# Kernel tuning notes

Measured on AMD Instinct MI355X. Metric: run time of the kernel, lower is better.

## Reference

```python
import jax, jax.numpy as jnp
import numpy as np

N = 50000      # nodes
E = 600000     # message-passing edges (avg degree 12)
P = 500000     # candidate pairs
DH = 128       # d_h
NRBF = 16      # n_rbf
NL = 3         # n_layers
RBF_MAX = 1.5  # coords in [0,1]^2 -> max dist sqrt(2) ~ 1.414


def _mlp2(x, W1, b1, W2, b2):
    # mlp([a, b, c]) = Linear(a,b) -> ReLU -> Linear(b,c); dropout=0.0 is a no-op
    return jnp.dot(jax.nn.relu(jnp.dot(x, W1) + b1), W2) + b2


def _rbf(r):
    # Gaussian radial basis expansion of edge distances, NRBF centers on [0, RBF_MAX]
    centers = jnp.linspace(0.0, RBF_MAX, NRBF, dtype=r.dtype)
    width = centers[1] - centers[0]
    return jnp.exp(-jnp.square((r[:, None] - centers) / width))


def setup_inputs() -> dict:
    key = jax.random.key(0)
    ks = jax.random.split(key, 24)

    def lin(k, fan_in, fan_out):
        return jax.random.normal(k, (fan_in, fan_out), dtype=jnp.float32) / np.sqrt(fan_in)

    def lin_stack(k, n, fan_in, fan_out):
        return jax.random.normal(k, (n, fan_in, fan_out), dtype=jnp.float32) / np.sqrt(fan_in)

    inp = {}
    inp["coords01"] = jax.random.uniform(ks[0], (N, 2), dtype=jnp.float32)
    inp["msg_edge_index"] = jax.random.randint(ks[1], (2, E), 0, N)
    inp["cand_pairs_uv"] = jax.random.randint(ks[2], (P, 2), 0, N)
    # node_in: mlp([2, DH, DH])
    inp["node_W1"] = lin(ks[3], 2, DH)
    inp["node_b1"] = jnp.zeros((DH,), jnp.float32)
    inp["node_W2"] = lin(ks[4], DH, DH)
    inp["node_b2"] = jnp.zeros((DH,), jnp.float32)
    # per-layer InvariantMPNN params, stacked over NL layers
    # message MLP: [2*DH + NRBF, DH, DH]
    inp["msg_W1"] = lin_stack(ks[5], NL, 2 * DH + NRBF, DH)
    inp["msg_b1"] = jnp.zeros((NL, DH), jnp.float32)
    inp["msg_W2"] = lin_stack(ks[6], NL, DH, DH)
    inp["msg_b2"] = jnp.zeros((NL, DH), jnp.float32)
    # update MLP: [2*DH, DH, DH]
    inp["upd_W1"] = lin_stack(ks[7], NL, 2 * DH, DH)
    inp["upd_b1"] = jnp.zeros((NL, DH), jnp.float32)
    inp["upd_W2"] = lin_stack(ks[8], NL, DH, DH)
    inp["upd_b2"] = jnp.zeros((NL, DH), jnp.float32)
    # edge head: mlp([2*DH + 1, DH, 1])
    inp["head_W1"] = lin(ks[9], 2 * DH + 1, DH)
    inp["head_b1"] = jnp.zeros((DH,), jnp.float32)
    inp["head_W2"] = lin(ks[10], DH, 1)
    inp["head_b2"] = jnp.zeros((1,), jnp.float32)
    return inp


def reference(coords01, node_W1, node_b1, node_W2, node_b2,
              msg_W1, msg_b1, msg_W2, msg_b2,
              upd_W1, upd_b1, upd_W2, upd_b2,
              head_W1, head_b1, head_W2, head_b2,
              msg_edge_index, cand_pairs_uv):
    # node embedding from 2D coordinates
    h = _mlp2(coords01, node_W1, node_b1, node_W2, node_b2)  # [N, DH]

    src = msg_edge_index[0]
    dst = msg_edge_index[1]
    dx = coords01[src] - coords01[dst]                       # [E, 2]
    r = jnp.sqrt(jnp.sum(dx * dx, axis=-1) + 1e-8)           # [E]
    rbf = _rbf(r)                                            # [E, NRBF]

    # stacked invariant MPNN layers (residual)
    for l in range(NL):
        m_in = jnp.concatenate([h[src], h[dst], rbf], axis=-1)          # [E, 2*DH+NRBF]
        m = _mlp2(m_in, msg_W1[l], msg_b1[l], msg_W2[l], msg_b2[l])     # [E, DH]
        agg = jax.ops.segment_sum(m, dst, num_segments=N)               # [N, DH]
        u_in = jnp.concatenate([h, agg], axis=-1)                       # [N, 2*DH]
        h = h + _mlp2(u_in, upd_W1[l], upd_b1[l], upd_W2[l], upd_b2[l])

    # candidate edge scoring head
    u = cand_pairs_uv[:, 0]
    v = cand_pairs_uv[:, 1]
    dxc = coords01[u] - coords01[v]
    rc = jnp.sqrt(jnp.sum(dxc * dxc, axis=-1) + 1e-8)[:, None]          # [P, 1]
    edge_in = jnp.concatenate([h[u], h[v], rc], axis=-1)                # [P, 2*DH+1]
    logits = _mlp2(edge_in, head_W1, head_b1, head_W2, head_b2)[:, 0]   # [P]
    return logits
```

## Files before the change

kernel.cpp:

```cpp
#include <hip/hip_runtime.h>
#include <hip/hip_bf16.h>

#define NN 50000
#define NE 600000
#define NP 500000
#define DH 128
#define NRBF 16
#define NL 3

typedef __attribute__((ext_vector_type(8))) short bf16x8;
typedef __attribute__((ext_vector_type(4))) float f32x4;

__device__ __forceinline__ unsigned short f2b(float f){
  unsigned int u = __float_as_uint(f);
  u += 0x7fffu + ((u >> 16) & 1u);
  return (unsigned short)(u >> 16);
}
__device__ __forceinline__ float b2f(unsigned short u){
  return __uint_as_float(((unsigned)u) << 16);
}

__device__ __forceinline__ void zero_acc(f32x4 (&acc)[4][2]){
#pragma unroll
  for (int i=0;i<4;i++)
#pragma unroll
    for (int j=0;j<2;j++)
#pragma unroll
      for (int r=0;r<4;r++) acc[i][j][r]=0.f;
}

template<int RSB, int KB>
__device__ __forceinline__ void gemm_sw(const short* X, const short* __restrict__ Bp,
                                        int t, f32x4 (&acc)[4][2]){
  const int lane=t&63, w=t>>6, m=lane&15, g=lane>>4;
  const char* Xc = (const char*)X;
#pragma unroll
  for (int kb=0; kb<KB; kb++){
    bf16x8 a[4];
#pragma unroll
    for (int rt=0; rt<4; rt++){
      int ar = rt*16 + m;
      a[rt] = *reinterpret_cast<const bf16x8*>(Xc + ar*RSB + ((kb*64 + g*16) ^ ((ar&7)<<4)));
    }
#pragma unroll
    for (int c=0;c<2;c++){
      bf16x8 b = *reinterpret_cast<const bf16x8*>(Bp + ((size_t)((w*2+c)*KB+kb)*64 + lane)*8);
#pragma unroll
      for (int rt=0; rt<4; rt++)
        acc[rt][c] = __builtin_amdgcn_mfma_f32_16x16x32_bf16(a[rt], b, acc[rt][c], 0,0,0);
    }
  }
}

__global__ void pack_w_kernel(const float* __restrict__ W0, int Kr, int KB,
                              long wStride, long oStride, short* __restrict__ out0){
  int l = blockIdx.y;
  const float* W = W0 + (size_t)l*wStride;
  short* out = out0 + (size_t)l*oStride;
  int idx = blockIdx.x*256 + threadIdx.x;
  int total = 8*KB*64;
  if (idx >= total) return;
  int lane = idx & 63;
  int kb = (idx>>6) % KB;
  int ct = (idx>>6) / KB;
  int col = ct*16 + (lane&15);
  int k0 = kb*32 + 8*(lane>>4);
  bf16x8 pv;
#pragma unroll
  for (int e=0;e<8;e++){
    int k = k0+e;
    float f = (k<Kr) ? W[(size_t)k*DH + col] : 0.f;
    pv[e] = (short)f2b(f);
  }
  *reinterpret_cast<bf16x8*>(out + (size_t)idx*8) = pv;
}

__global__ void hist_kernel(const int* __restrict__ keys, int stride, int n,
                            int* __restrict__ cnt){
  int e = blockIdx.x*256 + threadIdx.x;
  if (e < n) atomicAdd(&cnt[keys[(size_t)e*stride]], 1);
}

__global__ void scan_kernel(const int* __restrict__ cnt, int total, int* __restrict__ rowptr){
  __shared__ int parts[1024];
  const int t = threadIdx.x;
  const int CH = (NN + 1023)/1024;
  int base = t*CH;
  int s = 0;
  for (int i=0;i<CH;i++){ int j=base+i; if (j<NN) s += cnt[j]; }
  parts[t] = s; __syncthreads();
  for (int off=1; off<1024; off<<=1){
    int v = (t>=off) ? parts[t-off] : 0;
    __syncthreads();
    parts[t] += v;
    __syncthreads();
  }
  int ex = (t==0) ? 0 : parts[t-1];
  for (int i=0;i<CH;i++){
    int j=base+i;
    if (j<NN){ rowptr[j] = ex; ex += cnt[j]; }
  }
  if (t==0) rowptr[NN] = total;
}

__global__ void scatter_kernel(const int* __restrict__ srcI, const int* __restrict__ dstI,
                               int* __restrict__ ofs, int* __restrict__ ssrc,
                               int* __restrict__ sdst){
  int e = blockIdx.x*256 + threadIdx.x;
  if (e >= NE) return;
  int d = dstI[e];
  int p = atomicAdd(&ofs[d], 1);
  ssrc[p] = srcI[e];
  sdst[p] = d;
}

__global__ void pair_scatter_kernel(const int* __restrict__ pairs, int* __restrict__ ofs,
                                    int* __restrict__ su, int* __restrict__ sv,
                                    int* __restrict__ sidx){
  int p = blockIdx.x*256 + threadIdx.x;
  if (p >= NP) return;
  int u = pairs[2*p], v = pairs[2*p+1];
  int pos = atomicAdd(&ofs[u], 1);
  su[pos] = u; sv[pos] = v; sidx[pos] = p;
}

__global__ void rbf_kernel(const float* __restrict__ coords, const int* __restrict__ srcI,
                           const int* __restrict__ dstI, short* __restrict__ rbfp){
  int e = blockIdx.x*256 + threadIdx.x;
  if (e >= NE) return;
  int s = srcI[e], d = dstI[e];
  float dx = coords[2*s]-coords[2*d];
  float dy = coords[2*s+1]-coords[2*d+1];
  float r = sqrtf(dx*dx + dy*dy + 1e-8f);
  bf16x8 v0, v1;
#pragma unroll
  for (int i=0;i<8;i++){
    float t0 = (r - 0.1f*i)*10.f;
    v0[i] = (short)f2b(expf(-t0*t0));
    float t1 = (r - 0.1f*(i+8))*10.f;
    v1[i] = (short)f2b(expf(-t1*t1));
  }
  *reinterpret_cast<bf16x8*>(rbfp + (size_t)e*NRBF) = v0;
  *reinterpret_cast<bf16x8*>(rbfp + (size_t)e*NRBF + 8) = v1;
}

__global__ __launch_bounds__(256, 2) void node_kernel(
    const float* __restrict__ coords, const float* __restrict__ W1, const float* __restrict__ b1,
    const short* __restrict__ W2p, const float* __restrict__ b2,
    float* __restrict__ h, short* __restrict__ hbf)
{
  __shared__ __align__(16) short X[64*128];
  const int t = threadIdx.x;
  const int n0 = blockIdx.x*64;
  {
    int row = t >> 2;
    int n = n0 + row;
    float c0=0.f, c1=0.f;
    if (n < NN){ c0 = coords[2*n]; c1 = coords[2*n+1]; }
    char* Xc = (char*)X;
#pragma unroll
    for (int i=0;i<32;i++){
      int col = (t&3)*32 + i;
      float y = fmaxf(c0*W1[col] + c1*W1[DH+col] + b1[col], 0.f);
      *reinterpret_cast<short*>(Xc + row*256 + ((col*2) ^ ((row&7)<<4))) = (short)f2b(y);
    }
  }
  __syncthreads();
  f32x4 acc[4][2]; zero_acc(acc);
  gemm_sw<256,4>(X, W2p, t, acc);
  const int lane=t&63, w=t>>6, m=lane&15, g=lane>>4;
  float b2v0=b2[w*32+m], b2v1=b2[w*32+16+m];
#pragma unroll
  for (int rt=0;rt<4;rt++){
#pragma unroll
    for (int c=0;c<2;c++){
      float bb = c? b2v1 : b2v0;
      int col = (w*2+c)*16 + m;
#pragma unroll
      for (int r=0;r<4;r++){
        int row = rt*16 + g*4 + r;
        int n = n0 + row;
        if (n < NN){
          float val = acc[rt][c][r] + bb;
          h[(size_t)n*DH + col] = val;
          hbf[(size_t)n*DH + col] = (short)f2b(val);
        }
      }
    }
  }
}

__global__ __launch_bounds__(256, 2) void nodegemm2_f32(
    const short* __restrict__ hbf,
    const short* __restrict__ WpA, const float* __restrict__ biasA, float* __restrict__ outA,
    const short* __restrict__ WpB, float* __restrict__ outB)
{
  const int t=threadIdx.x, lane=t&63, w=t>>6, m=lane&15, g=lane>>4;
  const int n0 = blockIdx.x*64;
  f32x4 accA[4][2], accB[4][2]; zero_acc(accA); zero_acc(accB);
#pragma unroll
  for (int kb=0;kb<4;kb++){
    bf16x8 a[4];
#pragma unroll
    for (int rt=0;rt<4;rt++){
      int n = n0 + rt*16 + m; if (n >= NN) n = NN-1;
      a[rt] = *reinterpret_cast<const bf16x8*>(hbf + (size_t)n*DH + kb*32 + g*8);
    }
#pragma unroll
    for (int c=0;c<2;c++){
      bf16x8 bA = *reinterpret_cast<const bf16x8*>(WpA + ((size_t)((w*2+c)*4+kb)*64 + lane)*8);
      bf16x8 bB = *reinterpret_cast<const bf16x8*>(WpB + ((size_t)((w*2+c)*4+kb)*64 + lane)*8);
#pragma unroll
      for (int rt=0;rt<4;rt++){
        accA[rt][c] = __builtin_amdgcn_mfma_f32_16x16x32_bf16(a[rt], bA, accA[rt][c], 0,0,0);
        accB[rt][c] = __builtin_amdgcn_mfma_f32_16x16x32_bf16(a[rt], bB, accB[rt][c], 0,0,0);
      }
    }
  }
#pragma unroll
  for (int rt=0;rt<4;rt++){
#pragma unroll
    for (int c=0;c<2;c++){
      int col = (w*2+c)*16 + m;
      float bb = biasA ? biasA[col] : 0.f;
#pragma unroll
      for (int r=0;r<4;r++){
        int n = n0 + rt*16 + g*4 + r;
        if (n < NN){
          outA[(size_t)n*DH + col] = accA[rt][c][r] + bb;
          outB[(size_t)n*DH + col] = accB[rt][c][r];
        }
      }
    }
  }
}

__global__ __launch_bounds__(256, 4) void msg_kernel(
    const float* __restrict__ hA, const float* __restrict__ hB,
    const short* __restrict__ rbfp,
    const int* __restrict__ ssrc, const int* __restrict__ sdst,
    const short* __restrict__ W1cp, const short* __restrict__ W2p,
    const float* __restrict__ b2, float* __restrict__ agg)
{
  __shared__ __align__(16) short X[64*128];
  __shared__ int srcl[64], dstl[64];
  const int t=threadIdx.x, lane=t&63, w=t>>6, m=lane&15, g=lane>>4;
  const int e0 = blockIdx.x*64;
  if (t < 64) srcl[t] = ssrc[e0+t];
  else if (t < 128) dstl[t-64] = sdst[e0+t-64];
  __syncthreads();

  f32x4 acc[4][2];
  {
    bf16x8 a[4];
#pragma unroll
    for (int rt=0;rt<4;rt++){
      if (g < 2)
        a[rt] = *reinterpret_cast<const bf16x8*>(rbfp + (size_t)(e0+rt*16+m)*NRBF + g*8);
      else {
        bf16x8 z;
#pragma unroll
        for (int e=0;e<8;e++) z[e]=0;
        a[rt]=z;
      }
    }
#pragma unroll
    for (int c=0;c<2;c++){
      bf16x8 b = *reinterpret_cast<const bf16x8*>(W1cp + ((size_t)(w*2+c)*64 + lane)*8);
      f32x4 z; z[0]=0.f; z[1]=0.f; z[2]=0.f; z[3]=0.f;
#pragma unroll
      for (int rt=0;rt<4;rt++)
        acc[rt][c] = __builtin_amdgcn_mfma_f32_16x16x32_bf16(a[rt], b, z, 0,0,0);
    }
  }
#pragma unroll
  for (int rt=0;rt<4;rt++){
#pragma unroll
    for (int r=0;r<4;r++){
      int row = rt*16 + g*4 + r;
      int s = srcl[row], d = dstl[row];
#pragma unroll
      for (int c=0;c<2;c++){
        int col = (w*2+c)*16 + m;
        acc[rt][c][r] += hA[(size_t)s*DH + col] + hB[(size_t)d*DH + col];
      }
    }
  }
  {
    char* Xc = (char*)X;
#pragma unroll
    for (int rt=0;rt<4;rt++){
#pragma unroll
      for (int c=0;c<2;c++){
        int col = (w*2+c)*16 + m;
#pragma unroll
        for (int r=0;r<4;r++){
          int row = rt*16 + g*4 + r;
          float y = fmaxf(acc[rt][c][r], 0.f);
          *reinterpret_cast<short*>(Xc + row*256 + ((col*2) ^ ((row&7)<<4))) = (short)f2b(y);
        }
      }
    }
  }
  __syncthreads();

  f32x4 acc2[4][2]; zero_acc(acc2);
  gemm_sw<256,4>(X, W2p, t, acc2);
  __syncthreads();

  float b2v0=b2[w*32+m], b2v1=b2[w*32+16+m];
  {
    char* Xc = (char*)X;
#pragma unroll
    for (int rt=0;rt<4;rt++){
#pragma unroll
      for (int c=0;c<2;c++){
        float bb = c? b2v1 : b2v0;
        int col = (w*2+c)*16 + m;
#pragma unroll
        for (int r=0;r<4;r++){
          int row = rt*16 + g*4 + r;
          *reinterpret_cast<short*>(Xc + row*256 + ((col*2) ^ ((row&7)<<4))) =
              (short)f2b(acc2[rt][c][r] + bb);
        }
      }
    }
  }
  __syncthreads();

  {
    const char* Xc = (const char*)X;
    int col = t & 127, half = t >> 7;
    int r0 = half*32, r1 = r0 + 32;
    float s = 0.f;
    int cur = dstl[r0];
    for (int row=r0; row<r1; row++){
      int d = dstl[row];
      if (d != cur){
        atomicAdd(&agg[(size_t)cur*DH + col], s);
        s = 0.f; cur = d;
      }
      s += b2f(*reinterpret_cast<const unsigned short*>(
               Xc + row*256 + ((col*2) ^ ((row&7)<<4))));
    }
    atomicAdd(&agg[(size_t)cur*DH + col], s);
  }
}

__global__ __launch_bounds__(256, 2) void upd_kernel(
    const short* __restrict__ hbfin, const float* __restrict__ agg,
    const short* __restrict__ W1p, const float* __restrict__ b1,
    const short* __restrict__ W2p, const float* __restrict__ b2,
    float* __restrict__ h, short* __restrict__ hbfout)
{
  __shared__ __align__(16) short X[64*256];
  const int t = threadIdx.x;
  const int n0 = blockIdx.x*64;
  char* Xc = (char*)X;
#pragma unroll
  for (int j=0;j<4;j++){
    int slot = j*256 + t;
    int lane16 = slot & 15, row = slot >> 4;
    int n = n0 + row;
    int nc = n < NN ? n : NN-1;
    bf16x8 v = *reinterpret_cast<const bf16x8*>(hbfin + (size_t)nc*DH + lane16*8);
    *reinterpret_cast<bf16x8*>(Xc + row*512 + ((lane16*16) ^ ((row&7)<<4))) = v;
    const float* ap = agg + (size_t)nc*DH + lane16*8;
    bf16x8 o;
#pragma unroll
    for (int e=0;e<8;e++) o[e] = (short)f2b(ap[e]);
    *reinterpret_cast<bf16x8*>(Xc + row*512 + ((256 + lane16*16) ^ ((row&7)<<4))) = o;
  }
  __syncthreads();

  f32x4 acc[4][2]; zero_acc(acc);
  gemm_sw<512,8>(X, W1p, t, acc);
  __syncthreads();

  const int lane=t&63, w=t>>6, m=lane&15, g=lane>>4;
  float b1v0=b1[w*32+m], b1v1=b1[w*32+16+m];
#pragma unroll
  for (int rt=0;rt<4;rt++){
#pragma unroll
    for (int c=0;c<2;c++){
      float bb = c? b1v1 : b1v0;
      int col = (w*2+c)*16 + m;
#pragma unroll
      for (int r=0;r<4;r++){
        int row = rt*16 + g*4 + r;
        float y = fmaxf(acc[rt][c][r] + bb, 0.f);
        *reinterpret_cast<short*>(Xc + row*256 + ((col*2) ^ ((row&7)<<4))) = (short)f2b(y);
      }
    }
  }
  __syncthreads();

  f32x4 acc2[4][2]; zero_acc(acc2);
  gemm_sw<256,4>(X, W2p, t, acc2);

  float b2v0=b2[w*32+m], b2v1=b2[w*32+16+m];
#pragma unroll
  for (int rt=0;rt<4;rt++){
#pragma unroll
    for (int c=0;c<2;c++){
      float bb = c? b2v1 : b2v0;
      int col = (w*2+c)*16 + m;
#pragma unroll
      for (int r=0;r<4;r++){
        int row = rt*16 + g*4 + r;
        int n = n0 + row;
        if (n < NN){
          float val = h[(size_t)n*DH + col] + acc2[rt][c][r] + bb;
          h[(size_t)n*DH + col] = val;
          hbfout[(size_t)n*DH + col] = (short)f2b(val);
        }
      }
    }
  }
}

__global__ __launch_bounds__(256, 2) void head_kernel(
    const float* __restrict__ hU, const float* __restrict__ hV,
    const float* __restrict__ coords,
    const int* __restrict__ su, const int* __restrict__ sv,
    const int* __restrict__ sidx,
    const float* __restrict__ w1r, const float* __restrict__ W2,
    const float* __restrict__ b2, float* __restrict__ out)
{
  const int t = threadIdx.x;
  const int l = t & 31;
  long p = (long)blockIdx.x*8 + (t>>5);
  int u = su[p], v = sv[p];
  float dx = coords[2*u]-coords[2*v], dy = coords[2*u+1]-coords[2*v+1];
  float rc = sqrtf(dx*dx + dy*dy + 1e-8f);
  f32x4 a  = *reinterpret_cast<const f32x4*>(hU + (size_t)u*DH + l*4);
  f32x4 bb = *reinterpret_cast<const f32x4*>(hV + (size_t)v*DH + l*4);
  f32x4 wr = *reinterpret_cast<const f32x4*>(w1r + l*4);
  f32x4 w2 = *reinterpret_cast<const f32x4*>(W2 + l*4);
  float s = 0.f;
#pragma unroll
  for (int i=0;i<4;i++){
    float y = fmaxf(a[i] + bb[i] + rc*wr[i], 0.f);
    s += y * w2[i];
  }
#pragma unroll
  for (int off=1; off<32; off<<=1)
    s += __shfl_xor(s, off, 32);
  if (l == 0) out[sidx[p]] = s + b2[0];
}

extern "C" void kernel_launch(void* const* d_in, const int* in_sizes, int n_in,
                              void* d_out, int out_size, void* d_ws, size_t ws_size,
                              hipStream_t stream)
{
  const float* coords  = (const float*)d_in[0];
  const int*   eidx    = (const int*)d_in[1];
  const int*   pairs   = (const int*)d_in[2];
  const float* node_W1 = (const float*)d_in[3];
  const float* node_b1 = (const float*)d_in[4];
  const float* node_W2 = (const float*)d_in[5];
  const float* node_b2 = (const float*)d_in[6];
  const float* msg_W1  = (const float*)d_in[7];
  const float* msg_b1  = (const float*)d_in[8];
  const float* msg_W2  = (const float*)d_in[9];
  const float* msg_b2  = (const float*)d_in[10];
  const float* upd_W1  = (const float*)d_in[11];
  const float* upd_b1  = (const float*)d_in[12];
  const float* upd_W2  = (const float*)d_in[13];
  const float* upd_b2  = (const float*)d_in[14];
  const float* head_W1 = (const float*)d_in[15];
  const float* head_b1 = (const float*)d_in[16];
  const float* head_W2 = (const float*)d_in[17];
  const float* head_b2 = (const float*)d_in[18];

  char* ws = (char*)d_ws;
  size_t off = 0;
  auto alloc = [&](size_t bytes)->void*{ void* p = ws + off; off += (bytes + 255) & ~(size_t)255; return p; };
  float* h      = (float*)alloc((size_t)NN*DH*4);
  short* hbf    = (short*)alloc((size_t)NN*DH*2);
  short* rbfp   = (short*)alloc((size_t)NE*NRBF*2);
  float* hA     = (float*)alloc((size_t)NN*DH*4);
  float* hB     = (float*)alloc((size_t)NN*DH*4);
  float* agg    = (float*)alloc((size_t)NN*DH*4);
  int*   ssrc   = (int*)alloc((size_t)NE*4);
  int*   sdst   = (int*)alloc((size_t)NE*4);
  int*   cnt    = (int*)alloc((size_t)NN*4);
  int*   rowptr = (int*)alloc((size_t)(NN+1)*4);
  int*   ofs    = (int*)alloc((size_t)NN*4);
  short* msgW1ap= (short*)alloc((size_t)NL*4*4096*2);
  short* msgW1bp= (short*)alloc((size_t)NL*4*4096*2);
  short* msgW1cp= (short*)alloc((size_t)NL*1*4096*2);
  short* msgW2p = (short*)alloc((size_t)NL*4*4096*2);
  short* updW1p = (short*)alloc((size_t)NL*8*4096*2);
  short* updW2p = (short*)alloc((size_t)NL*4*4096*2);
  short* headUp = (short*)alloc((size_t)4*4096*2);
  short* headVp = (short*)alloc((size_t)4*4096*2);
  short* nodeW2p= (short*)alloc((size_t)4*4096*2);

  const int* srcI = eidx;
  const int* dstI = eidx + NE;

  hipMemsetAsync(cnt, 0, (size_t)NN*4, stream);
  hist_kernel<<<(NE+255)/256, 256, 0, stream>>>(dstI, 1, NE, cnt);
  scan_kernel<<<1, 1024, 0, stream>>>(cnt, NE, rowptr);
  hipMemcpyAsync(ofs, rowptr, (size_t)NN*4, hipMemcpyDeviceToDevice, stream);
  scatter_kernel<<<(NE+255)/256, 256, 0, stream>>>(srcI, dstI, ofs, ssrc, sdst);

  rbf_kernel<<<(NE+255)/256, 256, 0, stream>>>(coords, ssrc, sdst, rbfp);

  {
    dim3 g4((8*4*64+255)/256, NL), g1((8*1*64+255)/256, NL), g8((8*8*64+255)/256, NL);
    pack_w_kernel<<<g4, 256, 0, stream>>>(msg_W1,          128, 4, (long)272*DH, 4*4096, msgW1ap);
    pack_w_kernel<<<g4, 256, 0, stream>>>(msg_W1 + 128*DH, 128, 4, (long)272*DH, 4*4096, msgW1bp);
    pack_w_kernel<<<g1, 256, 0, stream>>>(msg_W1 + 256*DH,  16, 1, (long)272*DH, 1*4096, msgW1cp);
    pack_w_kernel<<<g4, 256, 0, stream>>>(msg_W2, 128, 4, (long)DH*DH, 4*4096, msgW2p);
    pack_w_kernel<<<g8, 256, 0, stream>>>(upd_W1, 256, 8, (long)256*DH, 8*4096, updW1p);
    pack_w_kernel<<<g4, 256, 0, stream>>>(upd_W2, 128, 4, (long)DH*DH, 4*4096, updW2p);
    dim3 s4((8*4*64+255)/256, 1);
    pack_w_kernel<<<s4, 256, 0, stream>>>(head_W1,          128, 4, 0, 0, headUp);
    pack_w_kernel<<<s4, 256, 0, stream>>>(head_W1 + 128*DH, 128, 4, 0, 0, headVp);
    pack_w_kernel<<<s4, 256, 0, stream>>>(node_W2, 128, 4, 0, 0, nodeW2p);
  }

  node_kernel<<<(NN+63)/64, 256, 0, stream>>>(coords, node_W1, node_b1, nodeW2p, node_b2, h, hbf);

  const int NB = (NN+63)/64;
  for (int l=0; l<NL; l++){
    nodegemm2_f32<<<NB, 256, 0, stream>>>(hbf,
        msgW1ap + (size_t)l*4*4096, msg_b1 + l*DH, hA,
        msgW1bp + (size_t)l*4*4096, hB);
    hipMemsetAsync(agg, 0, (size_t)NN*DH*4, stream);
    msg_kernel<<<NE/64, 256, 0, stream>>>(hA, hB, rbfp, ssrc, sdst,
        msgW1cp + (size_t)l*1*4096, msgW2p + (size_t)l*4*4096, msg_b2 + l*DH, agg);
    upd_kernel<<<NB, 256, 0, stream>>>(hbf, agg,
        updW1p + (size_t)l*8*4096, upd_b1 + l*DH,
        updW2p + (size_t)l*4*4096, upd_b2 + l*DH, h, hbf);
  }

  int* su   = ssrc;
  int* sv   = sdst;
  int* sidx = (int*)rbfp;
  hipMemsetAsync(cnt, 0, (size_t)NN*4, stream);
  hist_kernel<<<(NP+255)/256, 256, 0, stream>>>(pairs, 2, NP, cnt);
  scan_kernel<<<1, 1024, 0, stream>>>(cnt, NP, rowptr);
  hipMemcpyAsync(ofs, rowptr, (size_t)NN*4, hipMemcpyDeviceToDevice, stream);
  pair_scatter_kernel<<<(NP+255)/256, 256, 0, stream>>>(pairs, ofs, su, sv, sidx);

  nodegemm2_f32<<<NB, 256, 0, stream>>>(hbf, headUp, head_b1, hA, headVp, hB);
  head_kernel<<<NP/8, 256, 0, stream>>>(hA, hB, coords, su, sv, sidx,
      head_W1 + 256*DH, head_W2, head_b2, (float*)d_out);
}
```

Baseline: 942.2 us.

## Replace single-block prefix scan with multi-block three-pass scan

Replaces the single 1024-thread scan, where each thread serially walked a contiguous chunk of counts, with a blocksum / partial-scan / final-scan sequence spread over about 49 blocks. The final pass writes both rowptr and ofs, which removes the device-to-device memcpy. The goal is to cut the serialized, poorly coalesced scan latency in both CSR builds. In exchange it adds two extra small kernel launches per scan.

New measurement: 781.6 us. 1.21x faster.

```diff
diff --git a/kernel.cpp b/kernel.cpp
--- a/kernel.cpp
+++ b/kernel.cpp
@@ -7,6 +7,7 @@
 #define DH 128
 #define NRBF 16
 #define NL 3
+#define SCAN_NBLK ((NN + 1023) / 1024)
 
 typedef __attribute__((ext_vector_type(8))) short bf16x8;
 typedef __attribute__((ext_vector_type(4))) float f32x4;
@@ -81,26 +82,44 @@
   if (e < n) atomicAdd(&cnt[keys[(size_t)e*stride]], 1);
 }
 
-__global__ void scan_kernel(const int* __restrict__ cnt, int total, int* __restrict__ rowptr){
-  __shared__ int parts[1024];
-  const int t = threadIdx.x;
-  const int CH = (NN + 1023)/1024;
-  int base = t*CH;
-  int s = 0;
-  for (int i=0;i<CH;i++){ int j=base+i; if (j<NN) s += cnt[j]; }
-  parts[t] = s; __syncthreads();
+__global__ void blocksum_kernel(const int* __restrict__ cnt, int* __restrict__ partial){
+  __shared__ int red[1024];
+  int t = threadIdx.x, i = blockIdx.x*1024 + t;
+  red[t] = (i < NN) ? cnt[i] : 0;
+  __syncthreads();
+  for (int off=512; off>0; off>>=1){
+    if (t < off) red[t] += red[t+off];
+    __syncthreads();
+  }
+  if (t == 0) partial[blockIdx.x] = red[0];
+}
+
+__global__ void scanpartial_kernel(int* __restrict__ partial){
+  if (threadIdx.x == 0){
+    int s = 0;
+    for (int b=0; b<SCAN_NBLK; b++){ int v = partial[b]; partial[b] = s; s += v; }
+  }
+}
+
+__global__ void scanfinal_kernel(const int* __restrict__ cnt, const int* __restrict__ partial,
+                                 int total, int* __restrict__ rowptr, int* __restrict__ ofs){
+  __shared__ int sc[1024];
+  int t = threadIdx.x, i = blockIdx.x*1024 + t;
+  int v = (i < NN) ? cnt[i] : 0;
+  sc[t] = v;
+  __syncthreads();
   for (int off=1; off<1024; off<<=1){
-    int v = (t>=off) ? parts[t-off] : 0;
+    int u = (t >= off) ? sc[t-off] : 0;
     __syncthreads();
-    parts[t] += v;
+    sc[t] += u;
     __syncthreads();
   }
-  int ex = (t==0) ? 0 : parts[t-1];
-  for (int i=0;i<CH;i++){
-    int j=base+i;
-    if (j<NN){ rowptr[j] = ex; ex += cnt[j]; }
-  }
-  if (t==0) rowptr[NN] = total;
+  if (i < NN){
+    int ex = partial[blockIdx.x] + sc[t] - v;
+    rowptr[i] = ex;
+    ofs[i] = ex;
+  }
+  if (blockIdx.x == 0 && t == 0) rowptr[NN] = total;
 }
 
 __global__ void scatter_kernel(const int* __restrict__ srcI, const int* __restrict__ dstI,
@@ -487,6 +506,7 @@
   int*   cnt    = (int*)alloc((size_t)NN*4);
   int*   rowptr = (int*)alloc((size_t)(NN+1)*4);
   int*   ofs    = (int*)alloc((size_t)NN*4);
+  int*   partial= (int*)alloc((size_t)SCAN_NBLK*4);
   short* msgW1ap= (short*)alloc((size_t)NL*4*4096*2);
   short* msgW1bp= (short*)alloc((size_t)NL*4*4096*2);
   short* msgW1cp= (short*)alloc((size_t)NL*1*4096*2);
@@ -502,8 +522,9 @@
 
   hipMemsetAsync(cnt, 0, (size_t)NN*4, stream);
   hist_kernel<<<(NE+255)/256, 256, 0, stream>>>(dstI, 1, NE, cnt);
-  scan_kernel<<<1, 1024, 0, stream>>>(cnt, NE, rowptr);
-  hipMemcpyAsync(ofs, rowptr, (size_t)NN*4, hipMemcpyDeviceToDevice, stream);
+  blocksum_kernel<<<SCAN_NBLK, 1024, 0, stream>>>(cnt, partial);
+  scanpartial_kernel<<<1, 64, 0, stream>>>(partial);
+  scanfinal_kernel<<<SCAN_NBLK, 1024, 0, stream>>>(cnt, partial, NE, rowptr, ofs);
   scatter_kernel<<<(NE+255)/256, 256, 0, stream>>>(srcI, dstI, ofs, ssrc, sdst);
 
   rbf_kernel<<<(NE+255)/256, 256, 0, stream>>>(coords, ssrc, sdst, rbfp);
@@ -542,8 +563,9 @@
   int* sidx = (int*)rbfp;
   hipMemsetAsync(cnt, 0, (size_t)NN*4, stream);
   hist_kernel<<<(NP+255)/256, 256, 0, stream>>>(pairs, 2, NP, cnt);
-  scan_kernel<<<1, 1024, 0, stream>>>(cnt, NP, rowptr);
-  hipMemcpyAsync(ofs, rowptr, (size_t)NN*4, hipMemcpyDeviceToDevice, stream);
+  blocksum_kernel<<<SCAN_NBLK, 1024, 0, stream>>>(cnt, partial);
+  scanpartial_kernel<<<1, 64, 0, stream>>>(partial);
+  scanfinal_kernel<<<SCAN_NBLK, 1024, 0, stream>>>(cnt, partial, NP, rowptr, ofs);
   pair_scatter_kernel<<<(NP+255)/256, 256, 0, stream>>>(pairs, ofs, su, sv, sidx);
 
   nodegemm2_f32<<<NB, 256, 0, stream>>>(hbf, headUp, head_b1, hA, headVp, hB);
```
